# Performance work log

Measured on AMD Instinct MI355X. Metric: run time of the kernel, lower is better.

## Reference

```python
import jax, jax.numpy as jnp
import numpy as np

N = 100000
E = 3200000
F_IN = 512
HID = 16
C = 40


def setup_inputs() -> dict:
    key = jax.random.key(0)
    ks = jax.random.split(key, 6)
    x = jax.random.normal(ks[0], (N, F_IN), dtype=jnp.float32)
    edge_index = jax.random.randint(ks[1], (2, E), 0, N, dtype=jnp.int64)
    edge_weight = jax.random.uniform(ks[2], (E,), dtype=jnp.float32)
    # Glorot-style init like PyG GCNConv
    W1 = jax.random.normal(ks[3], (F_IN, HID), dtype=jnp.float32) * (1.0 / np.sqrt(F_IN))
    b1 = jnp.zeros((HID,), dtype=jnp.float32)
    W2 = jax.random.normal(ks[4], (HID, C), dtype=jnp.float32) * (1.0 / np.sqrt(HID))
    b2 = jnp.zeros((C,), dtype=jnp.float32)
    return {"x": x, "edge_index": edge_index, "edge_weight": edge_weight,
            "W1": W1, "b1": b1, "W2": W2, "b2": b2}


def _gcn_conv(h, W, b, row, col, norm, num_nodes):
    # h: [N, Fin] -> [N, Fout];  out = D^-1/2 A D^-1/2 (h W) + b, no self loops
    h = h @ W                                           # [N, Fout]
    msg = norm[:, None] * h[row]                        # gather + scale, [E, Fout]
    agg = jax.ops.segment_sum(msg, col, num_segments=num_nodes)  # scatter-add
    return agg + b


def reference(x, edge_index, edge_weight, W1, b1, W2, b2):
    num_nodes = x.shape[0]
    row, col = edge_index[0], edge_index[1]
    # symmetric gcn normalization (add_self_loops=False)
    deg = jax.ops.segment_sum(edge_weight, col, num_segments=num_nodes)  # [N]
    deg_inv_sqrt = jnp.where(deg > 0, jax.lax.rsqrt(jnp.maximum(deg, 1e-30)), 0.0)
    norm = deg_inv_sqrt[row] * edge_weight * deg_inv_sqrt[col]           # [E]

    h = jax.nn.relu(_gcn_conv(x, W1, b1, row, col, norm, num_nodes))
    # dropout is identity in eval mode (training=False)
    h = _gcn_conv(h, W2, b2, row, col, norm, num_nodes)
    return jax.nn.log_softmax(h, axis=-1)
```

## Files before the change

kernel.cpp:

```cpp
#include <hip/hip_runtime.h>

typedef float floatx4_t __attribute__((ext_vector_type(4)));
typedef __bf16 bf16x8_t __attribute__((ext_vector_type(8)));
typedef short shortx8_t __attribute__((ext_vector_type(8)));
typedef unsigned long long ull;

__device__ __forceinline__ unsigned short f2bf_rne(float f) {
    unsigned u = __float_as_uint(f);
    unsigned r = u + 0x7FFFu + ((u >> 16) & 1u);
    return (unsigned short)(r >> 16);
}
__device__ __forceinline__ float bf2f(unsigned short h) {
    return __uint_as_float((unsigned)h << 16);
}

#define MAXB 2048
#define CHUNK 8192
#define CAP 3072

__global__ __launch_bounds__(256) void k_scatter(const int* __restrict__ row,
                                                 const int* __restrict__ col,
                                                 const float* __restrict__ ew,
                                                 int* __restrict__ gcnt,
                                                 ull* __restrict__ packed,
                                                 int E, int B) {
    __shared__ int h[MAXB];
    __shared__ int base[MAXB];
    int t = threadIdx.x;
    for (int i = t; i < B; i += 256) h[i] = 0;
    __syncthreads();
    int cbase = blockIdx.x * CHUNK;
#pragma unroll 4
    for (int k = 0; k < 32; ++k) {
        int e = cbase + k * 256 + t;
        if (e < E) atomicAdd(&h[col[e] >> 6], 1);
    }
    __syncthreads();
    for (int i = t; i < B; i += 256) {
        int c = h[i];
        base[i] = c ? atomicAdd(&gcnt[i], c) : 0;
    }
    __syncthreads();
#pragma unroll 2
    for (int k = 0; k < 32; ++k) {
        int e = cbase + k * 256 + t;
        if (e < E) {
            int c = col[e];
            int b = c >> 6;
            int pos = atomicAdd(&base[b], 1);
            if (pos < CAP) {
                ull hi = (ull)(unsigned)((row[e] << 6) | (c & 63)) << 32;
                packed[(size_t)b * CAP + pos] = hi | (unsigned)__float_as_uint(ew[e]);
            }
        }
    }
}

__global__ __launch_bounds__(256) void k_bsort(const int* __restrict__ gcnt,
                                               ull* __restrict__ packed,
                                               int* __restrict__ rbeg,
                                               int* __restrict__ rend,
                                               float* __restrict__ dis, int N) {
    __shared__ ull buf[CAP];
    __shared__ int cnt[64];
    __shared__ int cur[64];
    __shared__ float dacc[64];
    int t = threadIdx.x;
    if (t < 64) { cnt[t] = 0; dacc[t] = 0.f; }
    __syncthreads();
    int b = blockIdx.x;
    size_t gbase = (size_t)b * CAP;
    int szr = gcnt[b];
    int sz = szr < CAP ? szr : CAP;

    for (int j = t; j < sz; j += 256) {
        ull p = packed[gbase + j];
        buf[j] = p;
        int nd = (int)(p >> 32) & 63;
        atomicAdd(&cnt[nd], 1);
        atomicAdd(&dacc[nd], __uint_as_float((unsigned)p));
    }
    __syncthreads();
    if (t < 64) {
        int c = cnt[t];
        int x = c;
#pragma unroll
        for (int off = 1; off < 64; off <<= 1) {
            int y = __shfl_up(x, off);
            if (t >= off) x += y;
        }
        int off0 = x - c;
        cur[t] = off0;
        int g = b * 64 + t;
        if (g < N) {
            rbeg[g] = (int)gbase + off0;
            rend[g] = (int)gbase + off0 + c;
            float s = dacc[t];
            dis[g] = (s > 0.f) ? rsqrtf(s) : 0.f;
        }
    }
    __syncthreads();
    for (int j = t; j < sz; j += 256) {
        ull p = buf[j];
        int nd = (int)(p >> 32) & 63;
        int pos = atomicAdd(&cur[nd], 1);
        packed[gbase + pos] = p;
    }
}

__global__ __launch_bounds__(256) void k_gemm1(const float* __restrict__ x,
                                               const float* __restrict__ W1,
                                               const float* __restrict__ dis,
                                               unsigned short* __restrict__ h1s, int N) {
    const int lane = threadIdx.x & 63;
    const int wave = threadIdx.x >> 6;
    const int m = lane & 15;
    const int q = lane >> 4;
    const int base = blockIdx.x * 64 + wave * 16;

    shortx8_t bs[16];
#pragma unroll
    for (int c = 0; c < 16; ++c) {
#pragma unroll
        for (int j = 0; j < 8; ++j) {
            int k = c * 32 + q * 8 + j;
            bs[c][j] = (short)f2bf_rne(W1[k * 16 + m]);
        }
    }

    int row = base + m;
    if (row >= N) row = N - 1;
    const float* xr = x + (size_t)row * 512;

    floatx4_t acc = {0.f, 0.f, 0.f, 0.f};
#pragma unroll
    for (int c = 0; c < 16; ++c) {
        const float4 u0 = *(const float4*)(xr + c * 32 + q * 8);
        const float4 u1 = *(const float4*)(xr + c * 32 + q * 8 + 4);
        shortx8_t as;
        as[0] = (short)f2bf_rne(u0.x); as[1] = (short)f2bf_rne(u0.y);
        as[2] = (short)f2bf_rne(u0.z); as[3] = (short)f2bf_rne(u0.w);
        as[4] = (short)f2bf_rne(u1.x); as[5] = (short)f2bf_rne(u1.y);
        as[6] = (short)f2bf_rne(u1.z); as[7] = (short)f2bf_rne(u1.w);
        acc = __builtin_amdgcn_mfma_f32_16x16x32_bf16(
            __builtin_bit_cast(bf16x8_t, as),
            __builtin_bit_cast(bf16x8_t, bs[c]), acc, 0, 0, 0);
    }

#pragma unroll
    for (int r = 0; r < 4; ++r) {
        int node = base + q * 4 + r;
        if (node < N) h1s[(size_t)node * 16 + m] = f2bf_rne(acc[r] * dis[node]);
    }
}

__global__ __launch_bounds__(256) void k_agg1(const int* __restrict__ rbeg,
                                              const int* __restrict__ rend,
                                              const ull* __restrict__ packed,
                                              const float* __restrict__ dis,
                                              const unsigned short* __restrict__ h1s,
                                              const float* __restrict__ b1,
                                              unsigned short* __restrict__ hs, int N) {
    int wv = (blockIdx.x * 256 + threadIdx.x) >> 6;
    if (wv >= N) return;
    int lane = threadIdx.x & 63;
    int e4 = lane >> 4, f = lane & 15;
    int beg = rbeg[wv], end = rend[wv];
    float a0 = 0.f, a1 = 0.f;
    int i = beg + e4;
    for (; i + 4 < end; i += 8) {
        ull p0 = packed[i];
        ull p1 = packed[i + 4];
        int r0 = (int)(p0 >> 32) >> 6;
        int r1 = (int)(p1 >> 32) >> 6;
        a0 += __uint_as_float((unsigned)p0) * bf2f(h1s[(size_t)r0 * 16 + f]);
        a1 += __uint_as_float((unsigned)p1) * bf2f(h1s[(size_t)r1 * 16 + f]);
    }
    if (i < end) {
        ull p = packed[i];
        int r = (int)(p >> 32) >> 6;
        a0 += __uint_as_float((unsigned)p) * bf2f(h1s[(size_t)r * 16 + f]);
    }
    float a = a0 + a1;
    a += __shfl_xor(a, 16);
    a += __shfl_xor(a, 32);
    if (e4 == 0) {
        float dg = dis[wv];
        float v = dg * a + b1[f];
        v = (v > 0.f) ? v : 0.f;
        hs[(size_t)wv * 16 + f] = f2bf_rne(dg * v);
    }
}

__global__ __launch_bounds__(256) void k_agg2out(const int* __restrict__ rbeg,
                                                 const int* __restrict__ rend,
                                                 const ull* __restrict__ packed,
                                                 const float* __restrict__ dis,
                                                 const unsigned short* __restrict__ hs,
                                                 const float* __restrict__ W2,
                                                 const float* __restrict__ b2,
                                                 float* __restrict__ out, int N) {
    int wv = (blockIdx.x * 256 + threadIdx.x) >> 6;
    if (wv >= N) return;
    int lane = threadIdx.x & 63;
    int e4 = lane >> 4, f = lane & 15;
    int beg = rbeg[wv], end = rend[wv];
    float a0 = 0.f, a1 = 0.f;
    int i = beg + e4;
    for (; i + 4 < end; i += 8) {
        ull p0 = packed[i];
        ull p1 = packed[i + 4];
        int r0 = (int)(p0 >> 32) >> 6;
        int r1 = (int)(p1 >> 32) >> 6;
        a0 += __uint_as_float((unsigned)p0) * bf2f(hs[(size_t)r0 * 16 + f]);
        a1 += __uint_as_float((unsigned)p1) * bf2f(hs[(size_t)r1 * 16 + f]);
    }
    if (i < end) {
        ull p = packed[i];
        int r = (int)(p >> 32) >> 6;
        a0 += __uint_as_float((unsigned)p) * bf2f(hs[(size_t)r * 16 + f]);
    }
    float a = a0 + a1;
    a += __shfl_xor(a, 16);
    a += __shfl_xor(a, 32);

    float dg = dis[wv];
    int c = lane;
    int cc = (c < 40) ? c : 39;
    float z = 0.f;
#pragma unroll
    for (int fi = 0; fi < 16; ++fi) {
        float af = __shfl(a, fi);
        z += af * W2[fi * 40 + cc];
    }
    z = dg * z + b2[cc];

    float zm = (c < 40) ? z : -3.4e38f;
#pragma unroll
    for (int off = 1; off < 64; off <<= 1) zm = fmaxf(zm, __shfl_xor(zm, off));
    float ex = (c < 40) ? __expf(z - zm) : 0.f;
    float s = ex;
#pragma unroll
    for (int off = 1; off < 64; off <<= 1) s += __shfl_xor(s, off);
    float lse = zm + __logf(s);
    if (c < 40) out[(size_t)wv * 40 + c] = z - lse;
}

extern "C" void kernel_launch(void* const* d_in, const int* in_sizes, int n_in,
                              void* d_out, int out_size, void* d_ws, size_t ws_size,
                              hipStream_t stream) {
    const float* x  = (const float*)d_in[0];
    const int*   ei = (const int*)d_in[1];
    const float* ew = (const float*)d_in[2];
    const float* W1 = (const float*)d_in[3];
    const float* b1 = (const float*)d_in[4];
    const float* W2 = (const float*)d_in[5];
    const float* b2 = (const float*)d_in[6];

    const int N = in_sizes[0] / 512;
    const int E = in_sizes[2];
    const int* row = ei;
    const int* col = ei + E;
    const int B = (N + 63) >> 6;

    ull*   packed = (ull*)d_ws;
    int*   gcnt   = (int*)(packed + (size_t)B * CAP);
    int*   rbeg   = gcnt + B;
    int*   rend   = rbeg + N;
    float* dis    = (float*)(rend + N);
    unsigned short* h1s = (unsigned short*)(dis + N);
    unsigned short* hs  = h1s + (size_t)16 * N;

    hipMemsetAsync(gcnt, 0, (size_t)B * sizeof(int), stream);

    const int gC = (E + CHUNK - 1) / CHUNK;
    const int gW = (N * 64 + 255) / 256;

    k_scatter<<<gC, 256, 0, stream>>>(row, col, ew, gcnt, packed, E, B);
    k_bsort<<<B, 256, 0, stream>>>(gcnt, packed, rbeg, rend, dis, N);
    k_gemm1<<<(N + 63) / 64, 256, 0, stream>>>(x, W1, dis, h1s, N);
    k_agg1<<<gW, 256, 0, stream>>>(rbeg, rend, packed, dis, h1s, b1, hs, N);
    k_agg2out<<<gW, 256, 0, stream>>>(rbeg, rend, packed, dis, hs, W2, b2, (float*)d_out, N);
}
```

Measured before the change: 569.1 us.

## Fuse bucket sort with GEMM1, compress edge records to 32 bits, vectorize scatter

Merges the per-bucket sort kernel with the first dense projection into one kernel, so the degree normalization comes from shared memory and one launch goes away. Sorted edges are written to a new 32-bit array holding a 17-bit source index and a truncated bf16 edge weight, which halves the edge bytes both aggregation passes read. The scatter kernel now loads col, row and weight as 4-wide vectors, and node ranges are stored as int2. In exchange the edge weights lose precision, source indices must fit in 17 bits, and the sort kernel no longer buffers in shared memory, so it reads packed from global memory twice.

```diff
diff --git a/kernel.cpp b/kernel.cpp
--- a/kernel.cpp
+++ b/kernel.cpp
@@ -30,10 +30,19 @@
     for (int i = t; i < B; i += 256) h[i] = 0;
     __syncthreads();
     int cbase = blockIdx.x * CHUNK;
-#pragma unroll 4
-    for (int k = 0; k < 32; ++k) {
-        int e = cbase + k * 256 + t;
-        if (e < E) atomicAdd(&h[col[e] >> 6], 1);
+#pragma unroll 2
+    for (int k = 0; k < 8; ++k) {
+        int e = cbase + k * 1024 + t * 4;
+        if (e + 3 < E) {
+            int4 c4 = *(const int4*)(col + e);
+            atomicAdd(&h[c4.x >> 6], 1);
+            atomicAdd(&h[c4.y >> 6], 1);
+            atomicAdd(&h[c4.z >> 6], 1);
+            atomicAdd(&h[c4.w >> 6], 1);
+        } else {
+            for (int j = 0; j < 4; ++j)
+                if (e + j < E) atomicAdd(&h[col[e + j] >> 6], 1);
+        }
     }
     __syncthreads();
     for (int i = t; i < B; i += 256) {
@@ -42,29 +51,53 @@
     }
     __syncthreads();
 #pragma unroll 2
-    for (int k = 0; k < 32; ++k) {
-        int e = cbase + k * 256 + t;
-        if (e < E) {
-            int c = col[e];
-            int b = c >> 6;
-            int pos = atomicAdd(&base[b], 1);
-            if (pos < CAP) {
-                ull hi = (ull)(unsigned)((row[e] << 6) | (c & 63)) << 32;
-                packed[(size_t)b * CAP + pos] = hi | (unsigned)__float_as_uint(ew[e]);
+    for (int k = 0; k < 8; ++k) {
+        int e = cbase + k * 1024 + t * 4;
+        if (e + 3 < E) {
+            int4 c4 = *(const int4*)(col + e);
+            int4 r4 = *(const int4*)(row + e);
+            float4 w4 = *(const float4*)(ew + e);
+            int cs[4] = {c4.x, c4.y, c4.z, c4.w};
+            int rs[4] = {r4.x, r4.y, r4.z, r4.w};
+            float wsv[4] = {w4.x, w4.y, w4.z, w4.w};
+#pragma unroll
+            for (int j = 0; j < 4; ++j) {
+                int c = cs[j];
+                int b = c >> 6;
+                int pos = atomicAdd(&base[b], 1);
+                if (pos < CAP) {
+                    ull hi = (ull)(unsigned)((rs[j] << 6) | (c & 63)) << 32;
+                    packed[(size_t)b * CAP + pos] = hi | (unsigned)__float_as_uint(wsv[j]);
+                }
             }
-        }
-    }
-}
-
-__global__ __launch_bounds__(256) void k_bsort(const int* __restrict__ gcnt,
-                                               ull* __restrict__ packed,
-                                               int* __restrict__ rbeg,
-                                               int* __restrict__ rend,
-                                               float* __restrict__ dis, int N) {
-    __shared__ ull buf[CAP];
+        } else {
+            for (int j = 0; j < 4; ++j) {
+                if (e + j < E) {
+                    int c = col[e + j];
+                    int b = c >> 6;
+                    int pos = atomicAdd(&base[b], 1);
+                    if (pos < CAP) {
+                        ull hi = (ull)(unsigned)((row[e + j] << 6) | (c & 63)) << 32;
+                        packed[(size_t)b * CAP + pos] = hi | (unsigned)__float_as_uint(ew[e + j]);
+                    }
+                }
+            }
+        }
+    }
+}
+
+__global__ __launch_bounds__(256) void k_sortgemm(const int* __restrict__ gcnt,
+                                                  const ull* __restrict__ packed,
+                                                  unsigned* __restrict__ packed2,
+                                                  int2* __restrict__ rng,
+                                                  float* __restrict__ dis,
+                                                  const float* __restrict__ x,
+                                                  const float* __restrict__ W1,
+                                                  unsigned short* __restrict__ h1s, int N) {
     __shared__ int cnt[64];
     __shared__ int cur[64];
     __shared__ float dacc[64];
+    __shared__ float sdis[64];
     int t = threadIdx.x;
     if (t < 64) { cnt[t] = 0; dacc[t] = 0.f; }
     __syncthreads();
@@ -75,7 +108,6 @@
 
     for (int j = t; j < sz; j += 256) {
         ull p = packed[gbase + j];
-        buf[j] = p;
         int nd = (int)(p >> 32) & 63;
         atomicAdd(&cnt[nd], 1);
         atomicAdd(&dacc[nd], __uint_as_float((unsigned)p));
@@ -83,40 +115,38 @@
     __syncthreads();
     if (t < 64) {
         int c = cnt[t];
-        int x = c;
+        int xp = c;
 #pragma unroll
         for (int off = 1; off < 64; off <<= 1) {
-            int y = __shfl_up(x, off);
-            if (t >= off) x += y;
-        }
-        int off0 = x - c;
+            int y = __shfl_up(xp, off);
+            if (t >= off) xp += y;
+        }
+        int off0 = xp - c;
         cur[t] = off0;
+        float s = dacc[t];
+        float d = (s > 0.f) ? rsqrtf(s) : 0.f;
+        sdis[t] = d;
         int g = b * 64 + t;
         if (g < N) {
-            rbeg[g] = (int)gbase + off0;
-            rend[g] = (int)gbase + off0 + c;
-            float s = dacc[t];
-            dis[g] = (s > 0.f) ? rsqrtf(s) : 0.f;
+            rng[g] = make_int2((int)gbase + off0, (int)gbase + off0 + c);
+            dis[g] = d;
         }
     }
     __syncthreads();
     for (int j = t; j < sz; j += 256) {
-        ull p = buf[j];
+        ull p = packed[gbase + j];
         int nd = (int)(p >> 32) & 63;
+        int r = (int)(p >> 32) >> 6;
+        unsigned short wb = f2bf_rne(__uint_as_float((unsigned)p));
         int pos = atomicAdd(&cur[nd], 1);
-        packed[gbase + pos] = p;
-    }
-}
-
-__global__ __launch_bounds__(256) void k_gemm1(const float* __restrict__ x,
-                                               const float* __restrict__ W1,
-                                               const float* __restrict__ dis,
-                                               unsigned short* __restrict__ h1s, int N) {
-    const int lane = threadIdx.x & 63;
-    const int wave = threadIdx.x >> 6;
+        packed2[gbase + pos] = ((unsigned)r << 15) | (unsigned)wb;
+    }
+
+    const int lane = t & 63;
+    const int wave = t >> 6;
     const int m = lane & 15;
     const int q = lane >> 4;
-    const int base = blockIdx.x * 64 + wave * 16;
+    const int nbase = b * 64 + wave * 16;
 
     shortx8_t bs[16];
 #pragma unroll
@@ -128,9 +158,9 @@
         }
     }
 
-    int row = base + m;
-    if (row >= N) row = N - 1;
-    const float* xr = x + (size_t)row * 512;
+    int rowi = nbase + m;
+    if (rowi >= N) rowi = N - 1;
+    const float* xr = x + (size_t)rowi * 512;
 
     floatx4_t acc = {0.f, 0.f, 0.f, 0.f};
 #pragma unroll
@@ -149,14 +179,14 @@
 
 #pragma unroll
     for (int r = 0; r < 4; ++r) {
-        int node = base + q * 4 + r;
-        if (node < N) h1s[(size_t)node * 16 + m] = f2bf_rne(acc[r] * dis[node]);
-    }
-}
-
-__global__ __launch_bounds__(256) void k_agg1(const int* __restrict__ rbeg,
-                                              const int* __restrict__ rend,
-                                              const ull* __restrict__ packed,
+        int node = nbase + q * 4 + r;
+        if (node < N)
+            h1s[(size_t)node * 16 + m] = f2bf_rne(acc[r] * sdis[wave * 16 + q * 4 + r]);
+    }
+}
+
+__global__ __launch_bounds__(256) void k_agg1(const int2* __restrict__ rng,
+                                              const unsigned* __restrict__ packed2,
                                               const float* __restrict__ dis,
                                               const unsigned short* __restrict__ h1s,
                                               const float* __restrict__ b1,
@@ -165,21 +195,21 @@
     if (wv >= N) return;
     int lane = threadIdx.x & 63;
     int e4 = lane >> 4, f = lane & 15;
-    int beg = rbeg[wv], end = rend[wv];
+    int2 r2 = rng[wv];
+    int beg = r2.x, end = r2.y;
     float a0 = 0.f, a1 = 0.f;
     int i = beg + e4;
     for (; i + 4 < end; i += 8) {
-        ull p0 = packed[i];
-        ull p1 = packed[i + 4];
-        int r0 = (int)(p0 >> 32) >> 6;
-        int r1 = (int)(p1 >> 32) >> 6;
-        a0 += __uint_as_float((unsigned)p0) * bf2f(h1s[(size_t)r0 * 16 + f]);
-        a1 += __uint_as_float((unsigned)p1) * bf2f(h1s[(size_t)r1 * 16 + f]);
+        unsigned p0 = packed2[i];
+        unsigned p1 = packed2[i + 4];
+        int r0 = p0 >> 15, r1 = p1 >> 15;
+        a0 += __uint_as_float((p0 & 0x7FFFu) << 16) * bf2f(h1s[(size_t)r0 * 16 + f]);
+        a1 += __uint_as_float((p1 & 0x7FFFu) << 16) * bf2f(h1s[(size_t)r1 * 16 + f]);
     }
     if (i < end) {
-        ull p = packed[i];
-        int r = (int)(p >> 32) >> 6;
-        a0 += __uint_as_float((unsigned)p) * bf2f(h1s[(size_t)r * 16 + f]);
+        unsigned p = packed2[i];
+        int r = p >> 15;
+        a0 += __uint_as_float((p & 0x7FFFu) << 16) * bf2f(h1s[(size_t)r * 16 + f]);
     }
     float a = a0 + a1;
     a += __shfl_xor(a, 16);
@@ -192,9 +222,8 @@
     }
 }
 
-__global__ __launch_bounds__(256) void k_agg2out(const int* __restrict__ rbeg,
-                                                 const int* __restrict__ rend,
-                                                 const ull* __restrict__ packed,
+__global__ __launch_bounds__(256) void k_agg2out(const int2* __restrict__ rng,
+                                                 const unsigned* __restrict__ packed2,
                                                  const float* __restrict__ dis,
                                                  const unsigned short* __restrict__ hs,
                                                  const float* __restrict__ W2,
@@ -204,21 +233,21 @@
     if (wv >= N) return;
     int lane = threadIdx.x & 63;
     int e4 = lane >> 4, f = lane & 15;
-    int beg = rbeg[wv], end = rend[wv];
+    int2 r2 = rng[wv];
+    int beg = r2.x, end = r2.y;
     float a0 = 0.f, a1 = 0.f;
     int i = beg + e4;
     for (; i + 4 < end; i += 8) {
-        ull p0 = packed[i];
-        ull p1 = packed[i + 4];
-        int r0 = (int)(p0 >> 32) >> 6;
-        int r1 = (int)(p1 >> 32) >> 6;
-        a0 += __uint_as_float((unsigned)p0) * bf2f(hs[(size_t)r0 * 16 + f]);
-        a1 += __uint_as_float((unsigned)p1) * bf2f(hs[(size_t)r1 * 16 + f]);
+        unsigned p0 = packed2[i];
+        unsigned p1 = packed2[i + 4];
+        int r0 = p0 >> 15, r1 = p1 >> 15;
+        a0 += __uint_as_float((p0 & 0x7FFFu) << 16) * bf2f(hs[(size_t)r0 * 16 + f]);
+        a1 += __uint_as_float((p1 & 0x7FFFu) << 16) * bf2f(hs[(size_t)r1 * 16 + f]);
     }
     if (i < end) {
-        ull p = packed[i];
-        int r = (int)(p >> 32) >> 6;
-        a0 += __uint_as_float((unsigned)p) * bf2f(hs[(size_t)r * 16 + f]);
+        unsigned p = packed2[i];
+        int r = p >> 15;
+        a0 += __uint_as_float((p & 0x7FFFu) << 16) * bf2f(hs[(size_t)r * 16 + f]);
     }
     float a = a0 + a1;
     a += __shfl_xor(a, 16);
@@ -263,11 +292,11 @@
     const int* col = ei + E;
     const int B = (N + 63) >> 6;
 
-    ull*   packed = (ull*)d_ws;
-    int*   gcnt   = (int*)(packed + (size_t)B * CAP);
-    int*   rbeg   = gcnt + B;
-    int*   rend   = rbeg + N;
-    float* dis    = (float*)(rend + N);
+    ull*      packed  = (ull*)d_ws;
+    unsigned* packed2 = (unsigned*)(packed + (size_t)B * CAP);
+    int*      gcnt    = (int*)(packed2 + (size_t)B * CAP);
+    int2*     rng     = (int2*)(gcnt + B + (B & 1));
+    float*    dis     = (float*)(rng + N);
     unsigned short* h1s = (unsigned short*)(dis + N);
     unsigned short* hs  = h1s + (size_t)16 * N;
 
@@ -277,8 +306,7 @@
     const int gW = (N * 64 + 255) / 256;
 
     k_scatter<<<gC, 256, 0, stream>>>(row, col, ew, gcnt, packed, E, B);
-    k_bsort<<<B, 256, 0, stream>>>(gcnt, packed, rbeg, rend, dis, N);
-    k_gemm1<<<(N + 63) / 64, 256, 0, stream>>>(x, W1, dis, h1s, N);
-    k_agg1<<<gW, 256, 0, stream>>>(rbeg, rend, packed, dis, h1s, b1, hs, N);
-    k_agg2out<<<gW, 256, 0, stream>>>(rbeg, rend, packed, dis, hs, W2, b2, (float*)d_out, N);
-}
+    k_sortgemm<<<B, 256, 0, stream>>>(gcnt, packed, packed2, rng, dis, x, W1, h1s, N);
+    k_agg1<<<gW, 256, 0, stream>>>(rng, packed2, dis, h1s, b1, hs, N);
+    k_agg2out<<<gW, 256, 0, stream>>>(rng, packed2, dis, hs, W2, b2, (float*)d_out, N);
+}
```

After: 540.7 us. -5.0%, faster.
